# Performance work log

Measured on AMD Instinct MI355X. Metric: run time of the kernel, lower is better.

## Reference

```python
import jax, jax.numpy as jnp
import numpy as np
from jax.scipy.linalg import solve_triangular

B, T, D = 2, 8192, 1024
HEAD_DIM = 128
H = D // HEAD_DIM  # 8 heads
C = 64             # chunk size (hard-coded in the torch module)


def setup_inputs() -> dict:
    key = jax.random.key(0)
    k0, k1, k2, k3 = jax.random.split(key, 4)
    scale = 0.02
    return {
        "out": jax.random.normal(k0, (B, T, D), jnp.float32),
        "W_write": jax.random.normal(k1, (D, D), jnp.float32) * scale,   # proj_write.weight (out,in)
        "W_read": jax.random.normal(k2, (D, D), jnp.float32) * scale,    # proj_read.weight
        "W_beta": jax.random.normal(k3, (H, D), jnp.float32) * scale,    # proj_beta.weight
        "decay": jnp.full((H,), 4.6, jnp.float32),                        # decay parameter
    }


def reference(out, W_write, W_read, W_beta, decay):
    Bs, Ts, Ds = out.shape
    d = HEAD_DIM
    Hn = Ds // d
    x = out.astype(jnp.float32)

    # keys: L2-normalized per head (F.normalize, eps=1e-12)
    k = x.reshape(Bs, Ts, Hn, d)
    k = k / jnp.maximum(jnp.linalg.norm(k, axis=-1, keepdims=True), 1e-12)
    k = k.transpose(0, 2, 1, 3)                                   # (B,H,T,d)
    v = (x @ W_write.T).reshape(Bs, Ts, Hn, d).transpose(0, 2, 1, 3)
    beta = jax.nn.sigmoid(x @ W_beta.T).transpose(0, 2, 1)[..., None]  # (B,H,T,1)
    v = v * beta
    k_beta = k * beta

    pad = (-Ts) % C
    if pad:
        pw = ((0, 0), (0, 0), (0, pad), (0, 0))
        k, v, k_beta = (jnp.pad(a, pw) for a in (k, v, k_beta))
    Tp = k.shape[2]
    N = Tp // C

    log_gamma = jnp.log(jax.nn.sigmoid(decay))                     # (H,)
    pos = jnp.arange(C, dtype=jnp.float32)
    cum_decay = (pos + 1.0)[None, :] * log_gamma[:, None]          # (H,C)
    Ldiff = cum_decay[:, :, None] - cum_decay[:, None, :]
    L = jnp.tril(jnp.exp(jnp.tril(Ldiff)))                         # (H,C,C)
    decay_exp = jnp.exp(cum_decay)[None, :, None, :, None]         # (1,H,1,C,1)
    chunk_total_decay = jnp.exp(cum_decay[:, -1])[None, :, None, None]  # (1,H,1,1)
    dw = jnp.exp(cum_decay[:, -1:] - cum_decay)[None, :, :, None]  # (1,H,C,1)
    de = jnp.exp(cum_decay)[None, :, :, None]                      # (1,H,C,1)

    k = k.reshape(Bs, Hn, N, C, d)
    v = v.reshape(Bs, Hn, N, C, d)
    k_beta = k_beta.reshape(Bs, Hn, N, C, d)

    # UT transform: original loop computes A = (I - A0)^{-1} with A0 strictly lower
    A0 = jnp.tril(-(jnp.einsum('bhnid,bhnjd->bhnij', k_beta, k) * L[None, :, None]), -1)
    eye = jnp.eye(C, dtype=jnp.float32)
    M = eye - A0                                                    # unit-diag lower triangular
    A = solve_triangular(M, jnp.broadcast_to(eye, M.shape), lower=True, unit_diagonal=True)

    v = A @ v
    k_cumdecay = A @ (k_beta * decay_exp)

    # inter-chunk sequential recurrence over N chunks
    kc = k.transpose(2, 0, 1, 3, 4)            # (N,B,H,C,d)
    vc = v.transpose(2, 0, 1, 3, 4)
    kcd = k_cumdecay.transpose(2, 0, 1, 3, 4)

    def step(S, inp):
        k_i, v_i, kcd_i = inp                  # (B,H,C,d)
        attn = jnp.tril(jnp.einsum('bhid,bhjd->bhij', k_i, k_i) * L[None])
        v_new = v_i - kcd_i @ S
        o_i = (k_i * de) @ S + attn @ v_new
        S_new = chunk_total_decay * S + jnp.einsum('bhcd,bhce->bhde', k_i * dw, v_new)
        return S_new, o_i

    S0 = jnp.zeros((Bs, Hn, d, d), jnp.float32)
    _, o = jax.lax.scan(step, S0, (kc, vc, kcd))  # o: (N,B,H,C,d)

    o = o.transpose(1, 2, 0, 3, 4).reshape(Bs, Hn, Tp, d)
    o = o.transpose(0, 2, 1, 3).reshape(Bs, Tp, Ds)[:, :Ts]
    return out + (o @ W_read.T).astype(out.dtype)
```

## Files before the change

### kernel.cpp

```cpp
#include <hip/hip_runtime.h>
#include <stdint.h>

#define DEV static __device__ __forceinline__

typedef float          f32x4  __attribute__((ext_vector_type(4)));
typedef short          bf16x8 __attribute__((ext_vector_type(8)));
typedef unsigned short u16x4  __attribute__((ext_vector_type(4)));
typedef unsigned short u16x8  __attribute__((ext_vector_type(8)));

#define B_   2
#define T_   8192
#define D_   1024
#define H_   8
#define HD_  128
#define N_   128

DEV float dot4(const float4& a, const float4& b) {
    return a.x * b.x + a.y * b.y + a.z * b.z + a.w * b.w;
}
DEV unsigned short f2bf(float f) {
    union { float f; unsigned u; } v; v.f = f;
    unsigned r = (v.u + 0x7fffu + ((v.u >> 16) & 1u)) >> 16;
    return (unsigned short)r;
}
DEV float bf2f(unsigned short u) {
    union { unsigned u; float f; } v; v.u = ((unsigned)u) << 16;
    return v.f;
}
DEV void cvt4(const float4 v, u16x4* h, u16x4* l) {
    const float* p = (const float*)&v;
    #pragma unroll
    for (int i = 0; i < 4; ++i) {
        unsigned short hv = f2bf(p[i]);
        (*h)[i] = hv;
        (*l)[i] = f2bf(p[i] - bf2f(hv));
    }
}
DEV void bar_lgkm() {
    asm volatile("s_waitcnt lgkmcnt(0)" ::: "memory");
    __builtin_amdgcn_s_barrier();
}
DEV float4* r512(char* base, int r, int u) {
    return (float4*)(base + (r << 9) + ((u << 4) ^ ((r & 7) << 4)));
}
DEV float ld_sk(char* base, int c, int dk) {
    return *(float*)(base + (c << 9) + ((((dk >> 2) << 4) ^ ((c & 7) << 4)) + ((dk & 3) << 2)));
}

__launch_bounds__(256)
__global__ void split_kernel(const float* __restrict__ src,
                             unsigned short* __restrict__ h,
                             unsigned short* __restrict__ l) {
// ... 107 lines not shown
            #pragma unroll
            for (int mt = 0; mt < 4; ++mt)
                #pragma unroll
                for (int nt = 0; nt < 4; ++nt) {
                    acc[mt][nt] = __builtin_amdgcn_mfma_f32_16x16x32_bf16(aH[mt], bH[nt], acc[mt][nt], 0, 0, 0);
                    acc[mt][nt] = __builtin_amdgcn_mfma_f32_16x16x32_bf16(aH[mt], bL[nt], acc[mt][nt], 0, 0, 0);
                    acc[mt][nt] = __builtin_amdgcn_mfma_f32_16x16x32_bf16(aL[mt], bH[nt], acc[mt][nt], 0, 0, 0);
                }
        }
    }
    #pragma unroll
    for (int mt = 0; mt < 4; ++mt)
        #pragma unroll
        for (int r = 0; r < 4; ++r) {
            int m = bm * 128 + wm * 64 + mt * 16 + lk * 4 + r;
            int b = m >> 13, t = m & 8191;
            float bet = beta[(size_t)(b * H_ + bn) * T_ + t];
            size_t ob = ((size_t)(b * H_ + bn) * T_ + t) * HD_;
            #pragma unroll
            for (int nt = 0; nt < 4; ++nt)
                vb[ob + wn * 64 + nt * 16 + lr] = acc[mt][nt][r] * bet;
        }
}

__launch_bounds__(256, 2)
__global__ void chunk_kernel(const unsigned short* __restrict__ khi,
                             const unsigned short* __restrict__ klo,
                             float* __restrict__ vb,
                             const float* __restrict__ beta_g,
                             const float* __restrict__ decay,
                             unsigned short* __restrict__ attn_g,
                             unsigned short* __restrict__ kcdhi_g,
                             unsigned short* __restrict__ kcdlo_g,
                             unsigned short* __restrict__ kdwh_g,
                             unsigned short* __restrict__ kdwl_g) {
    extern __shared__ char cs[];
    char*  sk = cs;
    float* sa = (float*)(cs + 32768);
    float* sm = (float*)(cs + 49152);
    __shared__ float sb[64];
    __shared__ float swgt[64];

    int cid = blockIdx.x;
    int bh = cid >> 7, cn = cid & 127;
    int h = bh & 7;
    int tid = threadIdx.x;
    float dec = decay[h];
    float sg = 1.0f / (1.0f + expf(-dec));
    float lg = logf(sg);
    size_t base = (size_t)cid * 8192;

    #pragma unroll
    for (int lq = 0; lq < 4; ++lq) {
        int f = tid + lq * 256;
        int c = f >> 4, u0 = (f & 15) << 1;
        u16x8 hh = *(const u16x8*)(khi + base + (size_t)f * 8);
        u16x8 ll = *(const u16x8*)(klo + base + (size_t)f * 8);
        float4 v0 = {bf2f(hh[0]) + bf2f(ll[0]), bf2f(hh[1]) + bf2f(ll[1]),
                     bf2f(hh[2]) + bf2f(ll[2]), bf2f(hh[3]) + bf2f(ll[3])};
        float4 v1 = {bf2f(hh[4]) + bf2f(ll[4]), bf2f(hh[5]) + bf2f(ll[5]),
                     bf2f(hh[6]) + bf2f(ll[6]), bf2f(hh[7]) + bf2f(ll[7])};
        *r512(sk, c, u0)     = v0;
        *r512(sk, c, u0 + 1) = v1;
    }
    if (tid < 64) {
        float bv = beta_g[(size_t)bh * T_ + cn * 64 + tid];
        sb[tid] = bv;
        swgt[tid] = bv * expf((float)(tid + 1) * lg);
    }
    __syncthreads();

    int bi = tid >> 4, bj = tid & 15;
    float dacc[4][4] = {};
    for (int u = 0; u < 32; ++u) {
        float4 ka[4], kc[4];
        #pragma unroll
        for (int i = 0; i < 4; ++i) ka[i] = *r512(sk, bi * 4 + i, u);
        #pragma unroll
        for (int j = 0; j < 4; ++j) kc[j] = *r512(sk, bj + 16 * j, u);
        #pragma unroll
        for (int i = 0; i < 4; ++i)
            #pragma unroll
            for (int j = 0; j < 4; ++j)
                dacc[i][j] += dot4(ka[i], kc[j]);
    }
    size_t abase = (size_t)cid * 4096;
    #pragma unroll
    for (int i = 0; i < 4; ++i) {
        int gi = bi * 4 + i;
        #pragma unroll
        for (int j = 0; j < 4; ++j) {
            int gj = bj + 16 * j;
            float dv = dacc[i][j];
            float dfac = expf((float)(gi - gj) * lg);
            attn_g[abase + (size_t)gi * 64 + gj] = (gi >= gj) ? f2bf(dv * dfac) : (unsigned short)0;
            sm[gi * 64 + gj] = (gj < gi) ? sb[gi] * dv * dfac : ((gi == gj) ? 1.f : 0.f);
        }
    }
    __syncthreads();

    if (tid < 64) {
        int j = tid;
        for (int i = 0; i < j; ++i) sa[i * 64 + j] = 0.f;
        sa[j * 64 + j] = 1.f;
        for (int i = j + 1; i < 64; ++i) {
            float s = 0.f;
            for (int p = j; p < i; ++p) s += sm[i * 64 + p] * sa[p * 64 + j];
            sa[i * 64 + j] = -s;
        }
    }
    __syncthreads();

    int ti = tid >> 4, te = tid & 15;
    {
        float ko[4][8] = {};
        for (int p = 0; p < 64; ++p) {
            float w = swgt[p];
            float4 k0 = *r512(sk, p, te * 2);
            float4 k1 = *r512(sk, p, te * 2 + 1);
            float kv[8] = {k0.x, k0.y, k0.z, k0.w, k1.x, k1.y, k1.z, k1.w};
            float a0 = sa[(ti * 4 + 0) * 64 + p] * w;
            float a1 = sa[(ti * 4 + 1) * 64 + p] * w;
            float a2 = sa[(ti * 4 + 2) * 64 + p] * w;
            float a3 = sa[(ti * 4 + 3) * 64 + p] * w;
            #pragma unroll
            for (int e = 0; e < 8; ++e) {
                ko[0][e] = fmaf(a0, kv[e], ko[0][e]);
                ko[1][e] = fmaf(a1, kv[e], ko[1][e]);
                ko[2][e] = fmaf(a2, kv[e], ko[2][e]);
                ko[3][e] = fmaf(a3, kv[e], ko[3][e]);
            }
        }
        #pragma unroll
        for (int i = 0; i < 4; ++i) {
            u16x8 hh, ll;
            #pragma unroll
            for (int e = 0; e < 8; ++e) {
                float t = -ko[i][e];
                unsigned short hv = f2bf(t);
                hh[e] = hv;
                ll[e] = f2bf(t - bf2f(hv));
            }
            size_t off = base + (size_t)(ti * 4 + i) * 128 + te * 8;
            *(u16x8*)(kcdhi_g + off) = hh;
            *(u16x8*)(kcdlo_g + off) = ll;
        }
    }

    {
        int dk = tid >> 1, ch = (tid & 1) * 32;
        #pragma unroll
        for (int q = 0; q < 4; ++q) {
            u16x8 th, tl;
            #pragma unroll
            for (int j = 0; j < 8; ++j) {
                int c = ch + q * 8 + j;
                float kv = ld_sk(sk, c, dk) * expf((float)(63 - c) * lg);
                unsigned short hv = f2bf(kv);
                th[j] = hv;
                tl[j] = f2bf(kv - bf2f(hv));
            }
            size_t off = base + (size_t)dk * 64 + ch + q * 8;
            *(u16x8*)(kdwh_g + off) = th;
            if (kdwl_g) *(u16x8*)(kdwl_g + off) = tl;
        }
    }
    __syncthreads();

    #pragma unroll
    for (int lq = 0; lq < 8; ++lq) {
        int f = tid + lq * 256;
        int r = f >> 5, u = f & 31;
        *r512(sk, r, u) = ((const float4*)(vb + base))[f];
    }
    __syncthreads();

    {
        float vo[4][8] = {};
        for (int p = 0; p < 64; ++p) {
            float4 v0 = *r512(sk, p, te * 2);
            float4 v1 = *r512(sk, p, te * 2 + 1);
            float vv[8] = {v0.x, v0.y, v0.z, v0.w, v1.x, v1.y, v1.z, v1.w};
            float a0 = sa[(ti * 4 + 0) * 64 + p];
            float a1 = sa[(ti * 4 + 1) * 64 + p];
            float a2 = sa[(ti * 4 + 2) * 64 + p];
            float a3 = sa[(ti * 4 + 3) * 64 + p];
            #pragma unroll
            for (int e = 0; e < 8; ++e) {
                vo[0][e] = fmaf(a0, vv[e], vo[0][e]);
                vo[1][e] = fmaf(a1, vv[e], vo[1][e]);
                vo[2][e] = fmaf(a2, vv[e], vo[2][e]);
                vo[3][e] = fmaf(a3, vv[e], vo[3][e]);
            }
        }
        #pragma unroll
        for (int i = 0; i < 4; ++i) {
            float4 lo = {vo[i][0], vo[i][1], vo[i][2], vo[i][3]};
// ... 2 lines not shown
            *(float4*)(vb + off)     = lo;
            *(float4*)(vb + off + 4) = hi;
        }
    }
}

#define SCAN_PREFETCH(NCH, fH, fL, atA, vnA)                                          \
    {                                                                                 \
        size_t nb = ((size_t)bh * N_ + (NCH)) * 8192;                                 \
        size_t na = ((size_t)bh * N_ + (NCH)) * 4096;                                 \
        if (grp == 0) {                                                               \
            _Pragma("unroll")                                                         \
            for (int ks = 0; ks < 4; ++ks) {                                          \
                size_t off = nb + (size_t)(cw * 16 + lr) * 128 + ks * 32 + lk * 8;    \
                fH[ks] = *(const bf16x8*)(kcdh + off);                                \
                fL[ks] = *(const bf16x8*)(kcdl + off);                                \
            }                                                                         \
            _Pragma("unroll")                                                         \
            for (int r = 0; r < 4; ++r)                                               \
                vnA[r] = vb[nb + (size_t)(cw * 16 + lk * 4 + r) * 128 + e0 + lr];     \
        } else {                                                                      \
            _Pragma("unroll")                                                         \
            for (int ks = 0; ks < 4; ++ks) {                                          \
                size_t off = nb + (size_t)(cw * 16 + lr) * 128 + ks * 32 + lk * 8;    \
                fH[ks] = *(const bf16x8*)(khi + off);                                 \
                fL[ks] = *(const bf16x8*)(klo + off);                                 \
            }                                                                         \
            _Pragma("unroll")                                                         \
            for (int ks2 = 0; ks2 < 2; ++ks2)                                         \
                atA[ks2] = *(const bf16x8*)(att + na + (size_t)(cw * 16 + lr) * 64 + ks2 * 32 + lk * 8); \
        }                                                                             \
    }

#define SCAN_STEP(CN, fH, fL, atA, vnA)                                               \
    {                                                                                 \
        size_t cb8 = ((size_t)bh * N_ + (CN)) * 8192;                                 \
        bf16x8 tH[2], tL[2];                                                          \
        _Pragma("unroll")                                                             \
        for (int ks2 = 0; ks2 < 2; ++ks2) {                                           \
            size_t off = cb8 + (size_t)(w * 16 + lr) * 64 + ks2 * 32 + lk * 8;        \
            tH[ks2] = *(const bf16x8*)(kdwh + off);                                   \
            if (haveLo) tL[ks2] = *(const bf16x8*)(kdwl + off);                       \
        }                                                                             \
        {                                                                             \
            u16x4 h4, l4;                                                             \
            _Pragma("unroll")                                                         \
            for (int r = 0; r < 4; ++r) {                                             \
                unsigned short hv = f2bf(Sacc[r]);                                    \
                h4[r] = hv;                                                           \
                l4[r] = f2bf(Sacc[r] - bf2f(hv));                                     \
            }                                                                         \
            int unit = 2 * w + (lk >> 1);                                             \
            int off = lr * 256 + ((unit ^ (lr & 7)) << 4) + ((lk & 1) << 3);          \
            *(u16x4*)(SH + off) = h4;                                                 \
            *(u16x4*)(SL + off) = l4;                                                 \
        }                                                                             \
        bar_lgkm();                                                                   \
        bf16x8 BH[4], BL[4];                                                          \
        _Pragma("unroll")                                                             \
        for (int ks = 0; ks < 4; ++ks) {                                              \
            int off = lr * 256 + (((ks * 4 + lk) ^ (lr & 7)) << 4);                   \
            BH[ks] = *(const bf16x8*)(SH + off);                                      \
            BL[ks] = *(const bf16x8*)(SL + off);                                      \
        }                                                                             \
        f32x4 acc1, acc2;                                                             \
        if (grp == 0) {                                                               \
            acc1 = vnA; acc2 = (f32x4){0.f, 0.f, 0.f, 0.f};                           \
            __builtin_amdgcn_s_setprio(1);                                            \
            _Pragma("unroll")                                                         \
            for (int ks = 0; ks < 2; ++ks) {                                          \
                acc1 = __builtin_amdgcn_mfma_f32_16x16x32_bf16(fH[ks], BH[ks], acc1, 0, 0, 0);       \
                acc2 = __builtin_amdgcn_mfma_f32_16x16x32_bf16(fH[ks+2], BH[ks+2], acc2, 0, 0, 0);   \
                acc1 = __builtin_amdgcn_mfma_f32_16x16x32_bf16(fH[ks], BL[ks], acc1, 0, 0, 0);       \
                acc2 = __builtin_amdgcn_mfma_f32_16x16x32_bf16(fH[ks+2], BL[ks+2], acc2, 0, 0, 0);   \
                acc1 = __builtin_amdgcn_mfma_f32_16x16x32_bf16(fL[ks], BH[ks], acc1, 0, 0, 0);       \
                acc2 = __builtin_amdgcn_mfma_f32_16x16x32_bf16(fL[ks+2], BH[ks+2], acc2, 0, 0, 0);   \
// ... 14 lines not shown
            __builtin_amdgcn_s_setprio(1);                                            \
            _Pragma("unroll")                                                         \
            for (int ks = 0; ks < 2; ++ks) {                                          \
                acc1 = __builtin_amdgcn_mfma_f32_16x16x32_bf16(fH[ks], BH[ks], acc1, 0, 0, 0);       \
                acc2 = __builtin_amdgcn_mfma_f32_16x16x32_bf16(fH[ks+2], BH[ks+2], acc2, 0, 0, 0);   \
                acc1 = __builtin_amdgcn_mfma_f32_16x16x32_bf16(fH[ks], BL[ks], acc1, 0, 0, 0);       \
                acc2 = __builtin_amdgcn_mfma_f32_16x16x32_bf16(fH[ks+2], BL[ks+2], acc2, 0, 0, 0);   \
                acc1 = __builtin_amdgcn_mfma_f32_16x16x32_bf16(fL[ks], BH[ks], acc1, 0, 0, 0);       \
                acc2 = __builtin_amdgcn_mfma_f32_16x16x32_bf16(fL[ks+2], BH[ks+2], acc2, 0, 0, 0);   \
            }                                                                         \
            __builtin_amdgcn_s_setprio(0);                                            \
        }                                                                             \
        bar_lgkm();                                                                   \
        bf16x8 VHf[2], VLf[2];                                                        \
        _Pragma("unroll")                                                             \
        for (int ks2 = 0; ks2 < 2; ++ks2) {                                           \
            int off = lr * 128 + (((ks2 * 4 + lk) ^ (lr & 7)) << 4);                  \
            VHf[ks2] = *(const bf16x8*)(VH + off);                                    \
            VLf[ks2] = *(const bf16x8*)(VL + off);                                    \
        }                                                                             \
        if (grp == 1) {                                                               \
            f32x4 om;                                                                 \
            _Pragma("unroll")                                                         \
            for (int r = 0; r < 4; ++r) om[r] = (acc1[r] + acc2[r]) * dev4[r];        \
            _Pragma("unroll")                                                         \
            for (int ks2 = 0; ks2 < 2; ++ks2) {                                       \
                om = __builtin_amdgcn_mfma_f32_16x16x32_bf16(atA[ks2], VHf[ks2], om, 0, 0, 0);  \
                om = __builtin_amdgcn_mfma_f32_16x16x32_bf16(atA[ks2], VLf[ks2], om, 0, 0, 0);  \
            }                                                                         \
            _Pragma("unroll")                                                         \
            for (int r = 0; r < 4; ++r)                                               \
                vb[cb8 + (size_t)(cw * 16 + lk * 4 + r) * 128 + e0 + lr] = om[r];     \
        }                                                                             \
        if ((CN) + 2 < N_) SCAN_PREFETCH((CN) + 2, fH, fL, atA, vnA)                  \
        {                                                                             \
            _Pragma("unroll")                                                         \
            for (int r = 0; r < 4; ++r) Sacc[r] *= g64;                               \
            f32x4 tmp = (f32x4){0.f, 0.f, 0.f, 0.f};                                  \
            __builtin_amdgcn_s_setprio(1);                                            \
            Sacc = __builtin_amdgcn_mfma_f32_16x16x32_bf16(tH[0], VHf[0], Sacc, 0, 0, 0);  \
            tmp  = __builtin_amdgcn_mfma_f32_16x16x32_bf16(tH[1], VHf[1], tmp,  0, 0, 0);  \
            Sacc = __builtin_amdgcn_mfma_f32_16x16x32_bf16(tH[0], VLf[0], Sacc, 0, 0, 0);  \
            tmp  = __builtin_amdgcn_mfma_f32_16x16x32_bf16(tH[1], VLf[1], tmp,  0, 0, 0);  \
            if (haveLo) {                                                             \
                Sacc = __builtin_amdgcn_mfma_f32_16x16x32_bf16(tL[0], VHf[0], Sacc, 0, 0, 0);  \
                tmp  = __builtin_amdgcn_mfma_f32_16x16x32_bf16(tL[1], VHf[1], tmp,  0, 0, 0);  \
            }                                                                         \
            __builtin_amdgcn_s_setprio(0);                                            \
            _Pragma("unroll")                                                         \
            for (int r = 0; r < 4; ++r) Sacc[r] += tmp[r];                            \
        }                                                                             \
    }

__launch_bounds__(512, 1)
__global__ void scan_kernel(const unsigned short* __restrict__ khi,
                            const unsigned short* __restrict__ klo,
                            float* __restrict__ vb,
                            const unsigned short* __restrict__ kcdh,
                            const unsigned short* __restrict__ kcdl,
                            const unsigned short* __restrict__ att,
                            const unsigned short* __restrict__ kdwh,
                            const unsigned short* __restrict__ kdwl,
                            const float* __restrict__ decay) {
    __shared__ char SH[4096];
    __shared__ char SL[4096];
    __shared__ char VH[2048];
    __shared__ char VL[2048];

    int bid = blockIdx.x;
    int bh = ((bid >> 6) << 3) + (bid & 7);
    int strip = (bid >> 3) & 7;
    int e0 = strip * 16;
    int tid = threadIdx.x;
    int w = tid >> 6, l = tid & 63, lr = l & 15, lk = l >> 4;
    int grp = w >> 2, cw = w & 3;
    float dec = decay[bh & 7];
    float sg = 1.0f / (1.0f + expf(-dec));
    float lg = logf(sg);
    float g64 = expf(64.f * lg);
    float dev4[4];
    #pragma unroll
    for (int r = 0; r < 4; ++r)
        dev4[r] = expf((float)(cw * 16 + lk * 4 + r + 1) * lg);
    const bool haveLo = (kdwl != nullptr);

    f32x4 Sacc = (f32x4){0.f, 0.f, 0.f, 0.f};

    bf16x8 fHa[4], fLa[4], atAa[2];
    bf16x8 fHb[4], fLb[4], atAb[2];
    f32x4 vnAa, vnAb;

    SCAN_PREFETCH(0, fHa, fLa, atAa, vnAa)
    SCAN_PREFETCH(1, fHb, fLb, atAb, vnAb)

    for (int cn = 0; cn < N_; cn += 2) {
        SCAN_STEP(cn,     fHa, fLa, atAa, vnAa)
        SCAN_STEP(cn + 1, fHb, fLb, atAb, vnAb)
    }
}

__launch_bounds__(256, 2)
__global__ void final_kernel(const float* __restrict__ X,
                             const unsigned short* __restrict__ Wh,
                             const unsigned short* __restrict__ Wl,
                             const float* __restrict__ OB, float* __restrict__ out) {
    extern __shared__ char gs[];
    char* AH = gs;
    char* AL = gs + 16384;
    char* BH = gs + 32768;
    char* BL = gs + 49152;
    int bm = blockIdx.x, bn = blockIdx.y;
    int tid = threadIdx.x;
    int w = tid >> 6, lr = tid & 15, lk = (tid & 63) >> 4;
    int wm = w >> 1, wn = w & 1;

    f32x4 acc[4][4];
    #pragma unroll
    for (int i = 0; i < 4; ++i)
        #pragma unroll
        for (int j = 0; j < 4; ++j) acc[i][j] = (f32x4){0.f, 0.f, 0.f, 0.f};

    for (int kt = 0; kt < 16; ++kt) {
        int hh = kt >> 1, e0g = (kt & 1) * 64;
        __syncthreads();
        #pragma unroll
        for (int q = 0; q < 8; ++q) {
            int f = tid + q * 256;
            int row = f >> 4, kq = f & 15;
            int m = bm * 128 + row;
            int b = m >> 13, t = m & 8191;
// ... 42 lines not shown
    }
    #pragma unroll
    for (int mt = 0; mt < 4; ++mt)
        #pragma unroll
        for (int r = 0; r < 4; ++r) {
            int m = bm * 128 + wm * 64 + mt * 16 + lk * 4 + r;
            size_t xo = (size_t)m * D_ + bn * 128;
            #pragma unroll
            for (int nt = 0; nt < 4; ++nt) {
                int n = wn * 64 + nt * 16 + lr;
                out[xo + n] = X[xo + n] + acc[mt][nt][r];
            }
        }
}

extern "C" void kernel_launch(void* const* d_in, const int* in_sizes, int n_in,
                              void* d_out, int out_size, void* d_ws, size_t ws_size,
                              hipStream_t stream) {
    const float* X   = (const float*)d_in[0];
    const float* Ww  = (const float*)d_in[1];
    const float* Wr  = (const float*)d_in[2];
    const float* Wb  = (const float*)d_in[3];
    const float* dec = (const float*)d_in[4];

    char* ws = (char*)d_ws;
    unsigned short* khi  = (unsigned short*)(ws);
    unsigned short* klo  = (unsigned short*)(ws + 33554432);
    float*          vb   = (float*)(ws + 67108864);
    unsigned short* kcdh = (unsigned short*)(ws + 134217728);
    unsigned short* kcdl = (unsigned short*)(ws + 167772160);
    unsigned short* attn = (unsigned short*)(ws + 201326592);
    float*          beta = (float*)(ws + 218103808);
    unsigned short* kdwh = (unsigned short*)(ws + 218628096);
    unsigned short* kdwl = (ws_size >= 285736960ull)
                         ? (unsigned short*)(ws + 252182528)
                         : (unsigned short*)nullptr;
    if (ws_size < 252182528ull) return;

    unsigned short* Wwh = (unsigned short*)(ws + 134217728);
    unsigned short* Wwl = (unsigned short*)(ws + 136314880);
    unsigned short* Wrh = (unsigned short*)(ws + 201326592);
    unsigned short* Wrl = (unsigned short*)(ws + 203423744);

    hipFuncSetAttribute((const void*)vproj_kernel, hipFuncAttributeMaxDynamicSharedMemorySize, 65536);
    hipFuncSetAttribute((const void*)chunk_kernel, hipFuncAttributeMaxDynamicSharedMemorySize, 65536);
    hipFuncSetAttribute((const void*)final_kernel, hipFuncAttributeMaxDynamicSharedMemorySize, 65536);

    hipLaunchKernelGGL(prep_kernel, dim3(B_ * T_), dim3(256), 0, stream, X, Wb, khi, klo, beta);
    hipLaunchKernelGGL(split_kernel, dim3(512), dim3(256), 0, stream, Ww, Wwh, Wwl);
    hipLaunchKernelGGL(vproj_kernel, dim3(128, 8), dim3(256), 65536, stream, X, Wwh, Wwl, beta, vb);
    hipLaunchKernelGGL(chunk_kernel, dim3(B_ * H_ * N_), dim3(256), 65536, stream,
                       khi, klo, vb, beta, dec, attn, kcdh, kcdl, kdwh, kdwl);
    hipLaunchKernelGGL(scan_kernel, dim3(128), dim3(512), 0, stream,
                       khi, klo, vb, kcdh, kcdl, attn, kdwh, kdwl, dec);
    hipLaunchKernelGGL(split_kernel, dim3(512), dim3(256), 0, stream, Wr, Wrh, Wrl);
    hipLaunchKernelGGL(final_kernel, dim3(128, 8), dim3(256), 65536, stream, X, Wrh, Wrl, vb, (float*)d_out);
}
```

Baseline: 962.0 us.

## Parallelize chunk recurrence scan across segments with affine-map composition

Splits the sequential scan over 128 chunks into 8 segments of 16 chunks each. A first pass computes each segment's affine state transition, both the linear part (state propagated from an identity start) and the offset part (state from a zero start). A small kernel then composes these maps serially to get the starting state of every segment, and a third kernel reruns each segment's scan in parallel to produce the outputs. This raises parallelism from 128 blocks to over a thousand, at the cost of extra work and extra launches. It also drops the low-bf16 half of the k*dw split, which lowers precision in the state update.

```diff
diff --git a/kernel.cpp b/kernel.cpp
--- a/kernel.cpp
+++ b/kernel.cpp
@@ -191,8 +191,7 @@
                              unsigned short* __restrict__ attn_g,
                              unsigned short* __restrict__ kcdhi_g,
                              unsigned short* __restrict__ kcdlo_g,
-                             unsigned short* __restrict__ kdwh_g,
-                             unsigned short* __restrict__ kdwl_g) {
+                             unsigned short* __restrict__ kdwh_g) {
     extern __shared__ char cs[];
     char*  sk = cs;
     float* sa = (float*)(cs + 32768);
@@ -310,18 +309,14 @@
         int dk = tid >> 1, ch = (tid & 1) * 32;
         #pragma unroll
         for (int q = 0; q < 4; ++q) {
-            u16x8 th, tl;
+            u16x8 th;
             #pragma unroll
             for (int j = 0; j < 8; ++j) {
                 int c = ch + q * 8 + j;
                 float kv = ld_sk(sk, c, dk) * expf((float)(63 - c) * lg);
-                unsigned short hv = f2bf(kv);
-                th[j] = hv;
-                tl[j] = f2bf(kv - bf2f(hv));
+                th[j] = f2bf(kv);
             }
-            size_t off = base + (size_t)dk * 64 + ch + q * 8;
-            *(u16x8*)(kdwh_g + off) = th;
-            if (kdwl_g) *(u16x8*)(kdwl_g + off) = tl;
+            *(u16x8*)(kdwh_g + base + (size_t)dk * 64 + ch + q * 8) = th;
         }
     }
     __syncthreads();
@@ -390,16 +385,13 @@
         }                                                                             \
     }
 
-#define SCAN_STEP(CN, fH, fL, atA, vnA)                                               \
+#define SCAN_STEP(CN, LIM, fH, fL, atA, vnA)                                          \
     {                                                                                 \
         size_t cb8 = ((size_t)bh * N_ + (CN)) * 8192;                                 \
-        bf16x8 tH[2], tL[2];                                                          \
+        bf16x8 tH[2];                                                                 \
         _Pragma("unroll")                                                             \
-        for (int ks2 = 0; ks2 < 2; ++ks2) {                                           \
-            size_t off = cb8 + (size_t)(w * 16 + lr) * 64 + ks2 * 32 + lk * 8;        \
-            tH[ks2] = *(const bf16x8*)(kdwh + off);                                   \
-            if (haveLo) tL[ks2] = *(const bf16x8*)(kdwl + off);                       \
-        }                                                                             \
+        for (int ks2 = 0; ks2 < 2; ++ks2)                                             \
+            tH[ks2] = *(const bf16x8*)(kdwh + cb8 + (size_t)(w * 16 + lr) * 64 + ks2 * 32 + lk * 8); \
         {                                                                             \
             u16x4 h4, l4;                                                             \
             _Pragma("unroll")                                                         \
@@ -480,7 +472,7 @@
             for (int r = 0; r < 4; ++r)                                               \
                 vb[cb8 + (size_t)(cw * 16 + lk * 4 + r) * 128 + e0 + lr] = om[r];     \
         }                                                                             \
-        if ((CN) + 2 < N_) SCAN_PREFETCH((CN) + 2, fH, fL, atA, vnA)                  \
+        if ((CN) + 2 < (LIM)) SCAN_PREFETCH((CN) + 2, fH, fL, atA, vnA)               \
         {                                                                             \
             _Pragma("unroll")                                                         \
             for (int r = 0; r < 4; ++r) Sacc[r] *= g64;                               \
@@ -490,10 +482,98 @@
             tmp  = __builtin_amdgcn_mfma_f32_16x16x32_bf16(tH[1], VHf[1], tmp,  0, 0, 0);  \
             Sacc = __builtin_amdgcn_mfma_f32_16x16x32_bf16(tH[0], VLf[0], Sacc, 0, 0, 0);  \
             tmp  = __builtin_amdgcn_mfma_f32_16x16x32_bf16(tH[1], VLf[1], tmp,  0, 0, 0);  \
-            if (haveLo) {                                                             \
-                Sacc = __builtin_amdgcn_mfma_f32_16x16x32_bf16(tL[0], VHf[0], Sacc, 0, 0, 0);  \
-                tmp  = __builtin_amdgcn_mfma_f32_16x16x32_bf16(tL[1], VHf[1], tmp,  0, 0, 0);  \
-            }                                                                         \
+            __builtin_amdgcn_s_setprio(0);                                            \
+            _Pragma("unroll")                                                         \
+            for (int r = 0; r < 4; ++r) Sacc[r] += tmp[r];                            \
+        }                                                                             \
+    }
+
+#define AB_PREFETCH(NCH, fH, fL, vnA)                                                 \
+    if (grp == 0) {                                                                   \
+        size_t nb = ((size_t)bh * N_ + (NCH)) * 8192;                                 \
+        _Pragma("unroll")                                                             \
+        for (int ks = 0; ks < 4; ++ks) {                                              \
+            size_t off = nb + (size_t)(cw * 16 + lr) * 128 + ks * 32 + lk * 8;        \
+            fH[ks] = *(const bf16x8*)(kcdh + off);                                    \
+            fL[ks] = *(const bf16x8*)(kcdl + off);                                    \
+        }                                                                             \
+        if (!isA) {                                                                   \
+            _Pragma("unroll")                                                         \
+            for (int r = 0; r < 4; ++r)                                               \
+                vnA[r] = vb[nb + (size_t)(cw * 16 + lk * 4 + r) * 128 + e0 + lr];     \
+        }                                                                             \
+    }
+
+#define AB_STEP(CN, LIM, fH, fL, vnA)                                                 \
+    {                                                                                 \
+        size_t cb8 = ((size_t)bh * N_ + (CN)) * 8192;                                 \
+        bf16x8 tH[2];                                                                 \
+        _Pragma("unroll")                                                             \
+        for (int ks2 = 0; ks2 < 2; ++ks2)                                             \
+            tH[ks2] = *(const bf16x8*)(kdwh + cb8 + (size_t)(w * 16 + lr) * 64 + ks2 * 32 + lk * 8); \
+        {                                                                             \
+            u16x4 h4, l4;                                                             \
+            _Pragma("unroll")                                                         \
+            for (int r = 0; r < 4; ++r) {                                             \
+                unsigned short hv = f2bf(Sacc[r]);                                    \
+                h4[r] = hv;                                                           \
+                l4[r] = f2bf(Sacc[r] - bf2f(hv));                                     \
+            }                                                                         \
+            int unit = 2 * w + (lk >> 1);                                             \
+            int off = lr * 256 + ((unit ^ (lr & 7)) << 4) + ((lk & 1) << 3);          \
+            *(u16x4*)(SH + off) = h4;                                                 \
+            *(u16x4*)(SL + off) = l4;                                                 \
+        }                                                                             \
+        bar_lgkm();                                                                   \
+        if (grp == 0) {                                                               \
+            bf16x8 BH[4], BL[4];                                                      \
+            _Pragma("unroll")                                                         \
+            for (int ks = 0; ks < 4; ++ks) {                                          \
+                int off = lr * 256 + (((ks * 4 + lk) ^ (lr & 7)) << 4);               \
+                BH[ks] = *(const bf16x8*)(SH + off);                                  \
+                BL[ks] = *(const bf16x8*)(SL + off);                                  \
+            }                                                                         \
+            f32x4 acc1 = vnA, acc2 = (f32x4){0.f, 0.f, 0.f, 0.f};                     \
+            __builtin_amdgcn_s_setprio(1);                                            \
+            _Pragma("unroll")                                                         \
+            for (int ks = 0; ks < 2; ++ks) {                                          \
+                acc1 = __builtin_amdgcn_mfma_f32_16x16x32_bf16(fH[ks], BH[ks], acc1, 0, 0, 0);       \
+                acc2 = __builtin_amdgcn_mfma_f32_16x16x32_bf16(fH[ks+2], BH[ks+2], acc2, 0, 0, 0);   \
+                acc1 = __builtin_amdgcn_mfma_f32_16x16x32_bf16(fH[ks], BL[ks], acc1, 0, 0, 0);       \
+                acc2 = __builtin_amdgcn_mfma_f32_16x16x32_bf16(fH[ks+2], BL[ks+2], acc2, 0, 0, 0);   \
+                acc1 = __builtin_amdgcn_mfma_f32_16x16x32_bf16(fL[ks], BH[ks], acc1, 0, 0, 0);       \
+                acc2 = __builtin_amdgcn_mfma_f32_16x16x32_bf16(fL[ks+2], BH[ks+2], acc2, 0, 0, 0);   \
+            }                                                                         \
+            __builtin_amdgcn_s_setprio(0);                                            \
+            u16x4 h4, l4;                                                             \
+            _Pragma("unroll")                                                         \
+            for (int r = 0; r < 4; ++r) {                                             \
+                float vv = acc1[r] + acc2[r];                                         \
+                unsigned short hv = f2bf(vv);                                         \
+                h4[r] = hv; l4[r] = f2bf(vv - bf2f(hv));                              \
+            }                                                                         \
+            int cu = 2 * cw + (lk >> 1);                                              \
+            int off = lr * 128 + ((cu ^ (lr & 7)) << 4) + ((lk & 1) << 3);            \
+            *(u16x4*)(VH + off) = h4;  *(u16x4*)(VL + off) = l4;                      \
+        }                                                                             \
+        bar_lgkm();                                                                   \
+        bf16x8 VHf[2], VLf[2];                                                        \
+        _Pragma("unroll")                                                             \
+        for (int ks2 = 0; ks2 < 2; ++ks2) {                                           \
+            int off = lr * 128 + (((ks2 * 4 + lk) ^ (lr & 7)) << 4);                  \
+            VHf[ks2] = *(const bf16x8*)(VH + off);                                    \
+            VLf[ks2] = *(const bf16x8*)(VL + off);                                    \
+        }                                                                             \
+        if ((CN) + 2 < (LIM)) AB_PREFETCH((CN) + 2, fH, fL, vnA)                      \
+        {                                                                             \
+            _Pragma("unroll")                                                         \
+            for (int r = 0; r < 4; ++r) Sacc[r] *= g64;                               \
+            f32x4 tmp = (f32x4){0.f, 0.f, 0.f, 0.f};                                  \
+            __builtin_amdgcn_s_setprio(1);                                            \
+            Sacc = __builtin_amdgcn_mfma_f32_16x16x32_bf16(tH[0], VHf[0], Sacc, 0, 0, 0);  \
+            tmp  = __builtin_amdgcn_mfma_f32_16x16x32_bf16(tH[1], VHf[1], tmp,  0, 0, 0);  \
+            Sacc = __builtin_amdgcn_mfma_f32_16x16x32_bf16(tH[0], VLf[0], Sacc, 0, 0, 0);  \
+            tmp  = __builtin_amdgcn_mfma_f32_16x16x32_bf16(tH[1], VLf[1], tmp,  0, 0, 0);  \
             __builtin_amdgcn_s_setprio(0);                                            \
             _Pragma("unroll")                                                         \
             for (int r = 0; r < 4; ++r) Sacc[r] += tmp[r];                            \
@@ -508,7 +588,6 @@
                             const unsigned short* __restrict__ kcdl,
                             const unsigned short* __restrict__ att,
                             const unsigned short* __restrict__ kdwh,
-                            const unsigned short* __restrict__ kdwl,
                             const float* __restrict__ decay) {
     __shared__ char SH[4096];
     __shared__ char SL[4096];
@@ -530,20 +609,203 @@
     #pragma unroll
     for (int r = 0; r < 4; ++r)
         dev4[r] = expf((float)(cw * 16 + lk * 4 + r + 1) * lg);
-    const bool haveLo = (kdwl != nullptr);
 
     f32x4 Sacc = (f32x4){0.f, 0.f, 0.f, 0.f};
-
     bf16x8 fHa[4], fLa[4], atAa[2];
     bf16x8 fHb[4], fLb[4], atAb[2];
     f32x4 vnAa, vnAb;
 
     SCAN_PREFETCH(0, fHa, fLa, atAa, vnAa)
     SCAN_PREFETCH(1, fHb, fLb, atAb, vnAb)
-
     for (int cn = 0; cn < N_; cn += 2) {
-        SCAN_STEP(cn,     fHa, fLa, atAa, vnAa)
-        SCAN_STEP(cn + 1, fHb, fLb, atAb, vnAb)
+        SCAN_STEP(cn,     N_, fHa, fLa, atAa, vnAa)
+        SCAN_STEP(cn + 1, N_, fHb, fLb, atAb, vnAb)
+    }
+}
+
+__launch_bounds__(512, 1)
+__global__ void phaseAB_kernel(const unsigned short* __restrict__ khi,
+                               const float* __restrict__ vb,
+                               const unsigned short* __restrict__ kcdh,
+                               const unsigned short* __restrict__ kcdl,
+                               const unsigned short* __restrict__ kdwh,
+                               const float* __restrict__ decay,
+                               float* __restrict__ Aseg,
+                               float* __restrict__ Bseg) {
+    __shared__ char SH[4096];
+    __shared__ char SL[4096];
+    __shared__ char VH[2048];
+    __shared__ char VL[2048];
+
+    int bid = blockIdx.x;
+    int strip = bid & 7;
+    int r2 = bid >> 3;
+    int sl = r2 % 13;
+    int bh = r2 / 13;
+    bool isA = sl < 6;
+    int seg = isA ? (sl + 1) : (sl - 6);
+    int c0 = seg * 16;
+    int e0 = strip * 16;
+    int tid = threadIdx.x;
+    int w = tid >> 6, l = tid & 63, lr = l & 15, lk = l >> 4;
+    int grp = w >> 2, cw = w & 3;
+    float dec = decay[bh & 7];
+    float sg = 1.0f / (1.0f + expf(-dec));
+    float lg = logf(sg);
+    float g64 = expf(64.f * lg);
+
+    f32x4 Sacc;
+    #pragma unroll
+    for (int r = 0; r < 4; ++r)
+        Sacc[r] = (isA && (w * 16 + lk * 4 + r) == (e0 + lr)) ? 1.f : 0.f;
+
+    bf16x8 fHa[4], fLa[4], fHb[4], fLb[4];
+    f32x4 vnAa = (f32x4){0.f, 0.f, 0.f, 0.f};
+    f32x4 vnAb = (f32x4){0.f, 0.f, 0.f, 0.f};
+
+    AB_PREFETCH(c0, fHa, fLa, vnAa)
+    AB_PREFETCH(c0 + 1, fHb, fLb, vnAb)
+    for (int cn = c0; cn < c0 + 16; cn += 2) {
+        AB_STEP(cn,     c0 + 16, fHa, fLa, vnAa)
+        AB_STEP(cn + 1, c0 + 16, fHb, fLb, vnAb)
+    }
+    float* dst = isA ? (Aseg + ((size_t)bh * 6 + (seg - 1)) * 16384)
+                     : (Bseg + ((size_t)bh * 7 + seg) * 16384);
+    #pragma unroll
+    for (int r = 0; r < 4; ++r)
+        dst[(size_t)(w * 16 + lk * 4 + r) * 128 + e0 + lr] = Sacc[r];
+}
+
+__launch_bounds__(512, 1)
+__global__ void phaseB_kernel(const float* __restrict__ Aseg,
+                              float* __restrict__ Bseg) {
+    extern __shared__ char ps[];
+    char* AH = ps;
+    char* AL = ps + 32768;
+    char* SH = ps + 65536;
+    char* SL = ps + 69632;
+
+    int bid = blockIdx.x;
+    int strip = bid & 7;
+    int bh = bid >> 3;
+    int e0 = strip * 16;
+    int tid = threadIdx.x;
+    int w = tid >> 6, l = tid & 63, lr = l & 15, lk = l >> 4;
+
+    f32x4 Eacc;
+    {
+        const float* E0 = Bseg + ((size_t)bh * 7) * 16384;
+        #pragma unroll
+        for (int r = 0; r < 4; ++r)
+            Eacc[r] = E0[(size_t)(w * 16 + lk * 4 + r) * 128 + e0 + lr];
+    }
+
+    for (int s = 1; s <= 6; ++s) {
+        __syncthreads();
+        {
+            u16x4 h4, l4;
+            #pragma unroll
+            for (int r = 0; r < 4; ++r) {
+                unsigned short hv = f2bf(Eacc[r]);
+                h4[r] = hv;
+                l4[r] = f2bf(Eacc[r] - bf2f(hv));
+            }
+            int unit = 2 * w + (lk >> 1);
+            int off = lr * 256 + ((unit ^ (lr & 7)) << 4) + ((lk & 1) << 3);
+            *(u16x4*)(SH + off) = h4;
+            *(u16x4*)(SL + off) = l4;
+        }
+        const float* Ag = Aseg + ((size_t)bh * 6 + (s - 1)) * 16384;
+        #pragma unroll
+        for (int q = 0; q < 8; ++q) {
+            int f = tid + q * 512;
+            int row = f >> 5, i4 = f & 31;
+            float4 av = ((const float4*)Ag)[f];
+            u16x4 ah, al;
+            cvt4(av, &ah, &al);
+            int off = row * 256 + ((((i4 >> 1) ^ (row & 7))) << 4) + ((i4 & 1) << 3);
+            *(u16x4*)(AH + off) = ah;
+            *(u16x4*)(AL + off) = al;
+        }
+        __syncthreads();
+        const float* Bg = Bseg + ((size_t)bh * 7 + s) * 16384;
+        f32x4 C;
+        #pragma unroll
+        for (int r = 0; r < 4; ++r)
+            C[r] = Bg[(size_t)(w * 16 + lk * 4 + r) * 128 + e0 + lr];
+        #pragma unroll
+        for (int ks = 0; ks < 4; ++ks) {
+            int arow = w * 16 + lr;
+            int aoff = arow * 256 + (((ks * 4 + lk) ^ (arow & 7)) << 4);
+            bf16x8 aH = *(const bf16x8*)(AH + aoff);
+            bf16x8 aL = *(const bf16x8*)(AL + aoff);
+            int boff = lr * 256 + (((ks * 4 + lk) ^ (lr & 7)) << 4);
+            bf16x8 bH = *(const bf16x8*)(SH + boff);
+            bf16x8 bL = *(const bf16x8*)(SL + boff);
+            C = __builtin_amdgcn_mfma_f32_16x16x32_bf16(aH, bH, C, 0, 0, 0);
+            C = __builtin_amdgcn_mfma_f32_16x16x32_bf16(aH, bL, C, 0, 0, 0);
+            C = __builtin_amdgcn_mfma_f32_16x16x32_bf16(aL, bH, C, 0, 0, 0);
+        }
+        Eacc = C;
+        float* Bo = Bseg + ((size_t)bh * 7 + s) * 16384;
+        #pragma unroll
+        for (int r = 0; r < 4; ++r)
+            Bo[(size_t)(w * 16 + lk * 4 + r) * 128 + e0 + lr] = Eacc[r];
+    }
+}
+
+__launch_bounds__(512, 1)
+__global__ void phaseC_kernel(const unsigned short* __restrict__ khi,
+                              const unsigned short* __restrict__ klo,
+                              float* __restrict__ vb,
+                              const unsigned short* __restrict__ kcdh,
+                              const unsigned short* __restrict__ kcdl,
+                              const unsigned short* __restrict__ att,
+                              const unsigned short* __restrict__ kdwh,
+                              const float* __restrict__ decay,
+                              const float* __restrict__ Eseg) {
+    __shared__ char SH[4096];
+    __shared__ char SL[4096];
+    __shared__ char VH[2048];
+    __shared__ char VL[2048];
+
+    int bid = blockIdx.x;
+    int strip = bid & 7;
+    int seg = (bid >> 3) & 7;
+    int bh = bid >> 6;
+    int c0 = seg * 16;
+    int e0 = strip * 16;
+    int tid = threadIdx.x;
+    int w = tid >> 6, l = tid & 63, lr = l & 15, lk = l >> 4;
+    int grp = w >> 2, cw = w & 3;
+    float dec = decay[bh & 7];
+    float sg = 1.0f / (1.0f + expf(-dec));
+    float lg = logf(sg);
+    float g64 = expf(64.f * lg);
+    float dev4[4];
+    #pragma unroll
+    for (int r = 0; r < 4; ++r)
+        dev4[r] = expf((float)(cw * 16 + lk * 4 + r + 1) * lg);
+
+    f32x4 Sacc;
+    if (seg == 0) {
+        Sacc = (f32x4){0.f, 0.f, 0.f, 0.f};
+    } else {
+        const float* E = Eseg + ((size_t)bh * 7 + seg - 1) * 16384;
+        #pragma unroll
+        for (int r = 0; r < 4; ++r)
+            Sacc[r] = E[(size_t)(w * 16 + lk * 4 + r) * 128 + e0 + lr];
+    }
+
+    bf16x8 fHa[4], fLa[4], atAa[2];
+    bf16x8 fHb[4], fLb[4], atAb[2];
+    f32x4 vnAa, vnAb;
+
+    SCAN_PREFETCH(c0, fHa, fLa, atAa, vnAa)
+    SCAN_PREFETCH(c0 + 1, fHb, fLb, atAb, vnAb)
+    for (int cn = c0; cn < c0 + 16; cn += 2) {
+        SCAN_STEP(cn,     c0 + 16, fHa, fLa, atAa, vnAa)
+        SCAN_STEP(cn + 1, c0 + 16, fHb, fLb, atAb, vnAb)
     }
 }
 
@@ -652,9 +914,9 @@
     unsigned short* attn = (unsigned short*)(ws + 201326592);
     float*          beta = (float*)(ws + 218103808);
     unsigned short* kdwh = (unsigned short*)(ws + 218628096);
-    unsigned short* kdwl = (ws_size >= 285736960ull)
-                         ? (unsigned short*)(ws + 252182528)
-                         : (unsigned short*)nullptr;
+    float*          Aseg = (float*)(ws + 252182528);
+    float*          Bseg = (float*)(ws + 252182528 + 6291456);
+    const bool      par  = (ws_size >= 265814016ull);
     if (ws_size < 252182528ull) return;
 
     unsigned short* Wwh = (unsigned short*)(ws + 134217728);
@@ -664,15 +926,24 @@
 
     hipFuncSetAttribute((const void*)vproj_kernel, hipFuncAttributeMaxDynamicSharedMemorySize, 65536);
     hipFuncSetAttribute((const void*)chunk_kernel, hipFuncAttributeMaxDynamicSharedMemorySize, 65536);
+    hipFuncSetAttribute((const void*)phaseB_kernel, hipFuncAttributeMaxDynamicSharedMemorySize, 73728);
     hipFuncSetAttribute((const void*)final_kernel, hipFuncAttributeMaxDynamicSharedMemorySize, 65536);
 
     hipLaunchKernelGGL(prep_kernel, dim3(B_ * T_), dim3(256), 0, stream, X, Wb, khi, klo, beta);
     hipLaunchKernelGGL(split_kernel, dim3(512), dim3(256), 0, stream, Ww, Wwh, Wwl);
     hipLaunchKernelGGL(vproj_kernel, dim3(128, 8), dim3(256), 65536, stream, X, Wwh, Wwl, beta, vb);
     hipLaunchKernelGGL(chunk_kernel, dim3(B_ * H_ * N_), dim3(256), 65536, stream,
-                       khi, klo, vb, beta, dec, attn, kcdh, kcdl, kdwh, kdwl);
-    hipLaunchKernelGGL(scan_kernel, dim3(128), dim3(512), 0, stream,
-                       khi, klo, vb, kcdh, kcdl, attn, kdwh, kdwl, dec);
+                       khi, klo, vb, beta, dec, attn, kcdh, kcdl, kdwh);
+    if (par) {
+        hipLaunchKernelGGL(phaseAB_kernel, dim3(1664), dim3(512), 0, stream,
+                           khi, vb, kcdh, kcdl, kdwh, dec, Aseg, Bseg);
+        hipLaunchKernelGGL(phaseB_kernel, dim3(128), dim3(512), 73728, stream, Aseg, Bseg);
+        hipLaunchKernelGGL(phaseC_kernel, dim3(1024), dim3(512), 0, stream,
+                           khi, klo, vb, kcdh, kcdl, attn, kdwh, dec, Bseg);
+    } else {
+        hipLaunchKernelGGL(scan_kernel, dim3(128), dim3(512), 0, stream,
+                           khi, klo, vb, kcdh, kcdl, attn, kdwh, dec);
+    }
     hipLaunchKernelGGL(split_kernel, dim3(512), dim3(256), 0, stream, Wr, Wrh, Wrl);
     hipLaunchKernelGGL(final_kernel, dim3(128, 8), dim3(256), 65536, stream, X, Wrh, Wrl, vb, (float*)d_out);
 }
```

Measured after the change: 993.8 us. +3.3%, slower.

## Use MFMA for chunk K·K^T, drop kdw low part, overlap kdw with solve

Applied to the files above, without the earlier changes.

The chunk kernel's intra-chunk key Gram matrix moves from a scalar fp32 dot-product loop over LDS onto bf16 MFMA with a three-product hi/lo split, reading fragments straight from global memory. The kdw (decay-weighted key) tensor is now stored only as a bf16 high part, so the scan kernel drops its two extra MFMAs and loads per step. The kdw write is moved onto idle threads during the serial triangular solve and uses precomputed decay weights, and the sm matrix gets a padded stride of 65 to reduce LDS bank conflicts. Dropping the low part of kdw lowers precision in the state update and could affect accuracy.

```diff
diff --git a/kernel.cpp b/kernel.cpp
--- a/kernel.cpp
+++ b/kernel.cpp
@@ -15,9 +15,6 @@
 #define HD_  128
 #define N_   128
 
-DEV float dot4(const float4& a, const float4& b) {
-    return a.x * b.x + a.y * b.y + a.z * b.z + a.w * b.w;
-}
 DEV unsigned short f2bf(float f) {
     union { float f; unsigned u; } v; v.f = f;
     unsigned r = (v.u + 0x7fffu + ((v.u >> 16) & 1u)) >> 16;
@@ -191,19 +188,20 @@
                              unsigned short* __restrict__ attn_g,
                              unsigned short* __restrict__ kcdhi_g,
                              unsigned short* __restrict__ kcdlo_g,
-                             unsigned short* __restrict__ kdwh_g,
-                             unsigned short* __restrict__ kdwl_g) {
+                             unsigned short* __restrict__ kdwh_g) {
     extern __shared__ char cs[];
     char*  sk = cs;
     float* sa = (float*)(cs + 32768);
     float* sm = (float*)(cs + 49152);
     __shared__ float sb[64];
     __shared__ float swgt[64];
+    __shared__ float gamw[64];
 
     int cid = blockIdx.x;
     int bh = cid >> 7, cn = cid & 127;
     int h = bh & 7;
     int tid = threadIdx.x;
+    int w = tid >> 6, l = tid & 63, lr = l & 15, lk = l >> 4;
     float dec = decay[h];
     float sg = 1.0f / (1.0f + expf(-dec));
     float lg = logf(sg);
@@ -226,36 +224,49 @@
         float bv = beta_g[(size_t)bh * T_ + cn * 64 + tid];
         sb[tid] = bv;
         swgt[tid] = bv * expf((float)(tid + 1) * lg);
+        gamw[tid] = expf((float)(63 - tid) * lg);
+    }
+
+    bf16x8 aH[4], aL[4];
+    #pragma unroll
+    for (int ks = 0; ks < 4; ++ks) {
+        size_t off = base + (size_t)(w * 16 + lr) * 128 + ks * 32 + lk * 8;
+        aH[ks] = *(const bf16x8*)(khi + off);
+        aL[ks] = *(const bf16x8*)(klo + off);
+    }
+    f32x4 dacc[4];
+    #pragma unroll
+    for (int nt = 0; nt < 4; ++nt) {
+        bf16x8 bH[4], bL[4];
+        #pragma unroll
+        for (int ks = 0; ks < 4; ++ks) {
+            size_t off = base + (size_t)(nt * 16 + lr) * 128 + ks * 32 + lk * 8;
+            bH[ks] = *(const bf16x8*)(khi + off);
+            bL[ks] = *(const bf16x8*)(klo + off);
+        }
+        f32x4 C = (f32x4){0.f, 0.f, 0.f, 0.f};
+        #pragma unroll
+        for (int ks = 0; ks < 4; ++ks) {
+            C = __builtin_amdgcn_mfma_f32_16x16x32_bf16(aH[ks], bH[ks], C, 0, 0, 0);
+            C = __builtin_amdgcn_mfma_f32_16x16x32_bf16(aH[ks], bL[ks], C, 0, 0, 0);
+            C = __builtin_amdgcn_mfma_f32_16x16x32_bf16(aL[ks], bH[ks], C, 0, 0, 0);
+        }
+        dacc[nt] = C;
     }
     __syncthreads();
 
-    int bi = tid >> 4, bj = tid & 15;
-    float dacc[4][4] = {};
-    for (int u = 0; u < 32; ++u) {
-        float4 ka[4], kc[4];
-        #pragma unroll
-        for (int i = 0; i < 4; ++i) ka[i] = *r512(sk, bi * 4 + i, u);
-        #pragma unroll
-        for (int j = 0; j < 4; ++j) kc[j] = *r512(sk, bj + 16 * j, u);
-        #pragma unroll
-        for (int i = 0; i < 4; ++i)
-            #pragma unroll
-            for (int j = 0; j < 4; ++j)
-                dacc[i][j] += dot4(ka[i], kc[j]);
-    }
     size_t abase = (size_t)cid * 4096;
     #pragma unroll
-    for (int i = 0; i < 4; ++i) {
-        int gi = bi * 4 + i;
-        #pragma unroll
-        for (int j = 0; j < 4; ++j) {
-            int gj = bj + 16 * j;
-            float dv = dacc[i][j];
+    for (int nt = 0; nt < 4; ++nt)
+        #pragma unroll
+        for (int r = 0; r < 4; ++r) {
+            int gi = w * 16 + lk * 4 + r;
+            int gj = nt * 16 + lr;
+            float dv = dacc[nt][r];
             float dfac = expf((float)(gi - gj) * lg);
             attn_g[abase + (size_t)gi * 64 + gj] = (gi >= gj) ? f2bf(dv * dfac) : (unsigned short)0;
-            sm[gi * 64 + gj] = (gj < gi) ? sb[gi] * dv * dfac : ((gi == gj) ? 1.f : 0.f);
-        }
-    }
+            sm[gi * 65 + gj] = (gj < gi) ? sb[gi] * dv * dfac : ((gi == gj) ? 1.f : 0.f);
+        }
     __syncthreads();
 
     if (tid < 64) {
@@ -264,8 +275,20 @@
         sa[j * 64 + j] = 1.f;
         for (int i = j + 1; i < 64; ++i) {
             float s = 0.f;
-            for (int p = j; p < i; ++p) s += sm[i * 64 + p] * sa[p * 64 + j];
+            for (int p = j; p < i; ++p) s += sm[i * 65 + p] * sa[p * 64 + j];
             sa[i * 64 + j] = -s;
+        }
+    } else if (tid >= 128) {
+        int dk = tid - 128;
+        #pragma unroll
+        for (int q = 0; q < 8; ++q) {
+            u16x8 th;
+            #pragma unroll
+            for (int j = 0; j < 8; ++j) {
+                int c = q * 8 + j;
+                th[j] = f2bf(ld_sk(sk, c, dk) * gamw[c]);
+            }
+            *(u16x8*)(kdwh_g + base + (size_t)dk * 64 + q * 8) = th;
         }
     }
     __syncthreads();
@@ -274,14 +297,14 @@
     {
         float ko[4][8] = {};
         for (int p = 0; p < 64; ++p) {
-            float w = swgt[p];
+            float wq = swgt[p];
             float4 k0 = *r512(sk, p, te * 2);
             float4 k1 = *r512(sk, p, te * 2 + 1);
             float kv[8] = {k0.x, k0.y, k0.z, k0.w, k1.x, k1.y, k1.z, k1.w};
-            float a0 = sa[(ti * 4 + 0) * 64 + p] * w;
-            float a1 = sa[(ti * 4 + 1) * 64 + p] * w;
-            float a2 = sa[(ti * 4 + 2) * 64 + p] * w;
-            float a3 = sa[(ti * 4 + 3) * 64 + p] * w;
+            float a0 = sa[(ti * 4 + 0) * 64 + p] * wq;
+            float a1 = sa[(ti * 4 + 1) * 64 + p] * wq;
+            float a2 = sa[(ti * 4 + 2) * 64 + p] * wq;
+            float a3 = sa[(ti * 4 + 3) * 64 + p] * wq;
             #pragma unroll
             for (int e = 0; e < 8; ++e) {
                 ko[0][e] = fmaf(a0, kv[e], ko[0][e]);
@@ -303,25 +326,6 @@
             size_t off = base + (size_t)(ti * 4 + i) * 128 + te * 8;
             *(u16x8*)(kcdhi_g + off) = hh;
             *(u16x8*)(kcdlo_g + off) = ll;
-        }
-    }
-
-    {
-        int dk = tid >> 1, ch = (tid & 1) * 32;
-        #pragma unroll
-        for (int q = 0; q < 4; ++q) {
-            u16x8 th, tl;
-            #pragma unroll
-            for (int j = 0; j < 8; ++j) {
-                int c = ch + q * 8 + j;
-                float kv = ld_sk(sk, c, dk) * expf((float)(63 - c) * lg);
-                unsigned short hv = f2bf(kv);
-                th[j] = hv;
-                tl[j] = f2bf(kv - bf2f(hv));
-            }
-            size_t off = base + (size_t)dk * 64 + ch + q * 8;
-            *(u16x8*)(kdwh_g + off) = th;
-            if (kdwl_g) *(u16x8*)(kdwl_g + off) = tl;
         }
     }
     __syncthreads();
@@ -390,16 +394,13 @@
         }                                                                             \
     }
 
-#define SCAN_STEP(CN, fH, fL, atA, vnA)                                               \
+#define SCAN_STEP(CN, LIM, fH, fL, atA, vnA)                                          \
     {                                                                                 \
         size_t cb8 = ((size_t)bh * N_ + (CN)) * 8192;                                 \
-        bf16x8 tH[2], tL[2];                                                          \
+        bf16x8 tH[2];                                                                 \
         _Pragma("unroll")                                                             \
-        for (int ks2 = 0; ks2 < 2; ++ks2) {                                           \
-            size_t off = cb8 + (size_t)(w * 16 + lr) * 64 + ks2 * 32 + lk * 8;        \
-            tH[ks2] = *(const bf16x8*)(kdwh + off);                                   \
-            if (haveLo) tL[ks2] = *(const bf16x8*)(kdwl + off);                       \
-        }                                                                             \
+        for (int ks2 = 0; ks2 < 2; ++ks2)                                             \
+            tH[ks2] = *(const bf16x8*)(kdwh + cb8 + (size_t)(w * 16 + lr) * 64 + ks2 * 32 + lk * 8); \
         {                                                                             \
             u16x4 h4, l4;                                                             \
             _Pragma("unroll")                                                         \
@@ -480,7 +481,7 @@
             for (int r = 0; r < 4; ++r)                                               \
                 vb[cb8 + (size_t)(cw * 16 + lk * 4 + r) * 128 + e0 + lr] = om[r];     \
         }                                                                             \
-        if ((CN) + 2 < N_) SCAN_PREFETCH((CN) + 2, fH, fL, atA, vnA)                  \
+        if ((CN) + 2 < (LIM)) SCAN_PREFETCH((CN) + 2, fH, fL, atA, vnA)               \
         {                                                                             \
             _Pragma("unroll")                                                         \
             for (int r = 0; r < 4; ++r) Sacc[r] *= g64;                               \
@@ -490,10 +491,6 @@
             tmp  = __builtin_amdgcn_mfma_f32_16x16x32_bf16(tH[1], VHf[1], tmp,  0, 0, 0);  \
             Sacc = __builtin_amdgcn_mfma_f32_16x16x32_bf16(tH[0], VLf[0], Sacc, 0, 0, 0);  \
             tmp  = __builtin_amdgcn_mfma_f32_16x16x32_bf16(tH[1], VLf[1], tmp,  0, 0, 0);  \
-            if (haveLo) {                                                             \
-                Sacc = __builtin_amdgcn_mfma_f32_16x16x32_bf16(tL[0], VHf[0], Sacc, 0, 0, 0);  \
-                tmp  = __builtin_amdgcn_mfma_f32_16x16x32_bf16(tL[1], VHf[1], tmp,  0, 0, 0);  \
-            }                                                                         \
             __builtin_amdgcn_s_setprio(0);                                            \
             _Pragma("unroll")                                                         \
             for (int r = 0; r < 4; ++r) Sacc[r] += tmp[r];                            \
@@ -508,7 +505,6 @@
                             const unsigned short* __restrict__ kcdl,
                             const unsigned short* __restrict__ att,
                             const unsigned short* __restrict__ kdwh,
-                            const unsigned short* __restrict__ kdwl,
                             const float* __restrict__ decay) {
     __shared__ char SH[4096];
     __shared__ char SL[4096];
@@ -530,20 +526,17 @@
     #pragma unroll
     for (int r = 0; r < 4; ++r)
         dev4[r] = expf((float)(cw * 16 + lk * 4 + r + 1) * lg);
-    const bool haveLo = (kdwl != nullptr);
 
     f32x4 Sacc = (f32x4){0.f, 0.f, 0.f, 0.f};
-
     bf16x8 fHa[4], fLa[4], atAa[2];
     bf16x8 fHb[4], fLb[4], atAb[2];
     f32x4 vnAa, vnAb;
 
     SCAN_PREFETCH(0, fHa, fLa, atAa, vnAa)
     SCAN_PREFETCH(1, fHb, fLb, atAb, vnAb)
-
     for (int cn = 0; cn < N_; cn += 2) {
-        SCAN_STEP(cn,     fHa, fLa, atAa, vnAa)
-        SCAN_STEP(cn + 1, fHb, fLb, atAb, vnAb)
+        SCAN_STEP(cn,     N_, fHa, fLa, atAa, vnAa)
+        SCAN_STEP(cn + 1, N_, fHb, fLb, atAb, vnAb)
     }
 }
 
@@ -652,9 +645,6 @@
     unsigned short* attn = (unsigned short*)(ws + 201326592);
     float*          beta = (float*)(ws + 218103808);
     unsigned short* kdwh = (unsigned short*)(ws + 218628096);
-    unsigned short* kdwl = (ws_size >= 285736960ull)
-                         ? (unsigned short*)(ws + 252182528)
-                         : (unsigned short*)nullptr;
     if (ws_size < 252182528ull) return;
 
     unsigned short* Wwh = (unsigned short*)(ws + 134217728);
@@ -663,16 +653,16 @@
     unsigned short* Wrl = (unsigned short*)(ws + 203423744);
 
     hipFuncSetAttribute((const void*)vproj_kernel, hipFuncAttributeMaxDynamicSharedMemorySize, 65536);
-    hipFuncSetAttribute((const void*)chunk_kernel, hipFuncAttributeMaxDynamicSharedMemorySize, 65536);
+    hipFuncSetAttribute((const void*)chunk_kernel, hipFuncAttributeMaxDynamicSharedMemorySize, 65792);
     hipFuncSetAttribute((const void*)final_kernel, hipFuncAttributeMaxDynamicSharedMemorySize, 65536);
 
     hipLaunchKernelGGL(prep_kernel, dim3(B_ * T_), dim3(256), 0, stream, X, Wb, khi, klo, beta);
     hipLaunchKernelGGL(split_kernel, dim3(512), dim3(256), 0, stream, Ww, Wwh, Wwl);
     hipLaunchKernelGGL(vproj_kernel, dim3(128, 8), dim3(256), 65536, stream, X, Wwh, Wwl, beta, vb);
-    hipLaunchKernelGGL(chunk_kernel, dim3(B_ * H_ * N_), dim3(256), 65536, stream,
-                       khi, klo, vb, beta, dec, attn, kcdh, kcdl, kdwh, kdwl);
+    hipLaunchKernelGGL(chunk_kernel, dim3(B_ * H_ * N_), dim3(256), 65792, stream,
+                       khi, klo, vb, beta, dec, attn, kcdh, kcdl, kdwh);
     hipLaunchKernelGGL(scan_kernel, dim3(128), dim3(512), 0, stream,
-                       khi, klo, vb, kcdh, kcdl, attn, kdwh, kdwl, dec);
+                       khi, klo, vb, kcdh, kcdl, attn, kdwh, dec);
     hipLaunchKernelGGL(split_kernel, dim3(512), dim3(256), 0, stream, Wr, Wrh, Wrl);
     hipLaunchKernelGGL(final_kernel, dim3(128, 8), dim3(256), 65536, stream, X, Wrh, Wrl, vb, (float*)d_out);
 }
```

Result: no change. 944.9 us (-1.8%).
